# Kernel tuning notes

Hardware: AMD Instinct MI355X
Metric: run time of the kernel (lower is better)

The kernel has to match this reference:

```python
import jax, jax.numpy as jnp
import numpy as np

TAGSET = 50
T = TAGSET + 2      # tag_size incl START/STOP
START = T - 2       # START_TAG = -2
STOP = T - 1        # STOP_TAG = -1
NEG = -10000.0
B, S = 1024, 512


def _constrain(feats):
    # emissions to START/STOP are forbidden
    return feats.at[..., START].set(NEG).at[..., STOP].set(NEG)


def setup_inputs() -> dict:
    key = jax.random.key(0)
    kf, kl, kt, ktr = jax.random.split(key, 4)
    feats = jax.random.normal(kf, (B, S, T), jnp.float32)
    lengths = jax.random.randint(kl, (B,), S // 4, S + 1)
    mask = jnp.arange(S)[None, :] < lengths[:, None]  # bool prefix mask [B,S]
    tags = jax.random.randint(kt, (B, S), 0, TAGSET)
    # learned param: transitions with START/STOP constraints (as reset_parameters, but random base)
    transitions = 0.1 * jax.random.normal(ktr, (T, T), jnp.float32)
    transitions = transitions.at[:, START].set(NEG).at[STOP, :].set(NEG)
    return {"feats": feats, "mask": mask, "tags": tags, "transitions": transitions}


def reference(feats, mask, tags, transitions):
    del tags  # not used by Viterbi decode (forward)
    feats = _constrain(feats)
    b, s, t = feats.shape
    maskb = mask.astype(bool)
    lengths = jnp.maximum(maskb.sum(axis=1), 1)  # [B]

    alpha0 = transitions[START][None, :] + feats[:, 0]  # [B,T]

    def vstep(alpha, xs):
        f_t, m_t = xs  # [B,T], [B]
        scores = alpha[:, :, None] + transitions[None, :, :] + f_t[:, None, :]  # [B,T_prev,T_cur]
        nxt = scores.max(axis=1)
        bp = scores.argmax(axis=1).astype(jnp.int32)  # [B,T]
        alpha = jnp.where(m_t[:, None], nxt, alpha)
        return alpha, bp

    alpha, history = jax.lax.scan(
        vstep, alpha0, (feats[:, 1:].transpose(1, 0, 2), maskb[:, 1:].T)
    )  # history: [S-1,B,T]

    best_last = jnp.argmax(alpha + transitions[:, STOP][None, :], axis=1).astype(jnp.int32)  # [B]

    # pad so hist_pad[pos] == history[pos-1] for pos>=1
    hist_pad = jnp.concatenate([jnp.zeros((1, b, t), jnp.int32), history], axis=0)  # [S,B,T]

    def tb(ptr, xs):
        pos, bp = xs  # scalar, [B,T]
        ptr = jnp.where(pos == lengths - 1, best_last, ptr)
        tag = jnp.where(pos <= lengths - 1, ptr, 0)  # positions past length stay 0
        nxt = jnp.take_along_axis(bp, ptr[:, None], axis=1)[:, 0]
        ptr = jnp.where((pos >= 1) & (pos <= lengths - 1), nxt, ptr)
        return ptr, tag

    _, decoded = jax.lax.scan(tb, best_last, (jnp.arange(s), hist_pad), reverse=True)  # [S,B]
    return decoded.T  # [B,S] int32 best path
```

## Files before the change

kernel.cpp:

```cpp
#include <hip/hip_runtime.h>

#define TT 52
#define NT 50
#define START_TAG 50
#define STOP_TAG 51
#define BB 1024
#define SS 512
#define BPSTR 64

__device__ __forceinline__ int seq_len(const void* mask, int b, int j) {
    int cnt = 0;
    const unsigned* w = (const unsigned*)mask;
    unsigned w0 = w[0];
    unsigned w1 = w[1];
    if (w0 == 0x01010101u) {
        const unsigned char* m = (const unsigned char*)mask + (size_t)b * SS;
        for (int k = j; k < SS; k += 64) cnt += (m[k] != 0);
    } else if (w0 == 0x3f800000u) {
        const float* m = (const float*)mask + (size_t)b * SS;
        for (int k = j; k < SS; k += 64) cnt += (m[k] != 0.f);
    } else if (w1 == 1u) {
        const int* m = (const int*)mask + (size_t)b * SS;
        for (int k = j; k < SS; k += 64) cnt += (m[k] != 0);
    } else {
        const long long* m = (const long long*)mask + (size_t)b * SS;
        for (int k = j; k < SS; k += 64) cnt += (m[k] != 0);
    }
    for (int off = 32; off; off >>= 1) cnt += __shfl_xor(cnt, off, 64);
    return cnt > 0 ? cnt : 1;
}

#define DP_STEP(FREG, POSV)                                                       \
    {                                                                             \
        const int abits_ = __builtin_bit_cast(int, alpha);                        \
        float s_[NT];                                                             \
        _Pragma("unroll")                                                         \
        for (int i_ = 0; i_ < NT; ++i_)                                           \
            s_[i_] = __builtin_bit_cast(float,                                    \
                         __builtin_amdgcn_readlane(abits_, i_)) + tt[i_];         \
        float m_[17];                                                             \
        _Pragma("unroll")                                                         \
        for (int k_ = 0; k_ < 16; ++k_)                                           \
            m_[k_] = fmaxf(fmaxf(s_[3 * k_], s_[3 * k_ + 1]), s_[3 * k_ + 2]);    \
        m_[16] = fmaxf(s_[48], s_[49]);                                           \
        float n_[6];                                                              \
        _Pragma("unroll")                                                         \
        for (int k_ = 0; k_ < 5; ++k_)                                            \
            n_[k_] = fmaxf(fmaxf(m_[3 * k_], m_[3 * k_ + 1]), m_[3 * k_ + 2]);    \
        n_[5] = fmaxf(m_[15], m_[16]);                                            \
        float q0_ = fmaxf(fmaxf(n_[0], n_[1]), n_[2]);                            \
        float q1_ = fmaxf(fmaxf(n_[3], n_[4]), n_[5]);                            \
        float bv_ = fmaxf(q0_, q1_);                                              \
        wsb[(size_t)(POSV) * 64] = bv_;                                           \
        alpha = bv_ + (FREG);                                                     \
    }

#define FLD(P) fp[(size_t)((P) < SS ? (P) : SS - 1) * TT]

__global__ __launch_bounds__(64, 1) void crf_viterbi_fast(
    const float* __restrict__ feats,
    const void*  __restrict__ mask,
    const float* __restrict__ trans,
    float* __restrict__ ws,
    int* __restrict__ out)
{
    __shared__ float trans_lds[64 * 53];

    const int b = blockIdx.x;
    const int j = threadIdx.x;
    const int jc = j < NT ? j : NT - 1;
    const int jr = j * 53;

    for (int k = j; k < 64 * 53; k += 64) {
        int r = k / 53, c = k - r * 53;
        float v = -3.0e38f;
        if (r < NT && c < TT) v = trans[r * TT + c];
        trans_lds[k] = v;
    }

    const int len = seq_len(mask, b, j);

    float tt[NT];
#pragma unroll
    for (int i = 0; i < NT; ++i) tt[i] = trans[i * TT + j];

    const float* fp = feats + ((size_t)b * SS) * TT + jc;
    float* wsb = ws + ((size_t)b * SS) * 64 + j;
    const float bv0 = trans[START_TAG * TT + jc];
    float alpha = bv0 + fp[0];
    wsb[0] = bv0;

    float fA0 = FLD(1), fA1 = FLD(2), fA2 = FLD(3), fA3 = FLD(4);
    float fB0 = FLD(5), fB1 = FLD(6), fB2 = FLD(7), fB3 = FLD(8);

    int pos = 1;
    for (; pos + 7 < len; pos += 8) {
        DP_STEP(fA0, pos + 0)
        DP_STEP(fA1, pos + 1)
        DP_STEP(fA2, pos + 2)
        DP_STEP(fA3, pos + 3)
        fA0 = FLD(pos + 8);  fA1 = FLD(pos + 9);
        fA2 = FLD(pos + 10); fA3 = FLD(pos + 11);
        DP_STEP(fB0, pos + 4)
        DP_STEP(fB1, pos + 5)
        DP_STEP(fB2, pos + 6)
        DP_STEP(fB3, pos + 7)
        fB0 = FLD(pos + 12); fB1 = FLD(pos + 13);
        fB2 = FLD(pos + 14); fB3 = FLD(pos + 15);
    }
    if (pos < len) { DP_STEP(fA0, pos) ++pos; }
    if (pos < len) { DP_STEP(fA1, pos) ++pos; }
    if (pos < len) { DP_STEP(fA2, pos) ++pos; }
    if (pos < len) { DP_STEP(fA3, pos) ++pos; }
    if (pos < len) { DP_STEP(fB0, pos) ++pos; }
    if (pos < len) { DP_STEP(fB1, pos) ++pos; }
    if (pos < len) { DP_STEP(fB2, pos) ++pos; }

    float v = alpha + trans[jc * TT + STOP_TAG];
    if (j >= NT) v = -3.0e38f;
    int idx = j < NT ? j : 0;
    for (int off = 32; off; off >>= 1) {
        float vo = __shfl_xor(v, off, 64);
        int   io = __shfl_xor(idx, off, 64);
        if (vo > v || (vo == v && io < idx)) { v = vo; idx = io; }
    }

    __syncthreads();

    int ptr = idx;
    int* ob = out + (size_t)b * SS;
    ob[len - 1] = ptr;

    const float* wsr = ws + ((size_t)b * SS) * 64;
    const float* fbase = feats + ((size_t)b * SS) * TT;

    float bvs[4], fs[4];
    float bv_cur;
    {
        int r0 = len - 1;
        bv_cur = wsr[(size_t)r0 * 64 + j];
#pragma unroll
        for (int k = 0; k < 4; ++k) {
            int r = len - 2 - k; int rc = r < 0 ? 0 : r;
            bvs[k] = wsr[(size_t)rc * 64 + j];
            fs[k]  = fbase[(size_t)rc * TT + jc];
        }
    }

    int tpos = len - 1;

#define TB_STEP(k)                                                              \
    {                                                                           \
        float bv_prev = bvs[k];                                                 \
        float alpha_prev = bv_prev + fs[k];                                     \
        float cand = alpha_prev + trans_lds[jr + ptr];                          \
        float candm = (j < NT) ? cand : -3.0e38f;                               \
        float tgt = __builtin_bit_cast(float,                                   \
            __builtin_amdgcn_readlane(__builtin_bit_cast(int, bv_cur), ptr));   \
        unsigned long long bm = __ballot(candm == tgt);                         \
        ptr = __ffsll(bm) - 1;                                                  \
        --tpos;                                                                 \
        ob[tpos] = ptr;                                                         \
        bv_cur = bv_prev;                                                       \
        int rc = tpos - 4; rc = rc < 0 ? 0 : rc;                                \
        bvs[k] = wsr[(size_t)rc * 64 + j];                                      \
        fs[k]  = fbase[(size_t)rc * TT + jc];                                   \
    }

    while (tpos >= 4) {
        TB_STEP(0) TB_STEP(1) TB_STEP(2) TB_STEP(3)
    }
#pragma unroll
    for (int k = 0; k < 3; ++k) {
        if (tpos >= 1) TB_STEP(k)
    }
#undef TB_STEP

    for (int p = len + j; p < SS; p += 64) ob[p] = 0;
}

__global__ __launch_bounds__(64, 1) void crf_viterbi(
    const float* __restrict__ feats,
    const void*  __restrict__ mask,
    const float* __restrict__ trans,
    int* __restrict__ out)
{
    __shared__ unsigned char bp_sh[SS * BPSTR];

    const int b = blockIdx.x;
    const int j = threadIdx.x;
    const int jc = j < NT ? j : NT - 1;

    const int len = seq_len(mask, b, j);

    float tt[NT];
#pragma unroll
    for (int i = 0; i < NT; ++i) tt[i] = trans[i * TT + j];

    const float* fp = feats + ((size_t)b * SS) * TT + jc;
    float alpha = trans[START_TAG * TT + jc] + fp[0];
    float fnext = fp[TT];

    for (int pos = 1; pos < len; ++pos) {
        const float f = fnext;
        { int np = pos + 1 < SS ? pos + 1 : SS - 1; fnext = fp[(size_t)np * TT]; }

        float best[4] = { -3.0e38f, -3.0e38f, -3.0e38f, -3.0e38f };
        int   bidx[4] = { 0, 0, 0, 0 };
        const int abits = __builtin_bit_cast(int, alpha);
#pragma unroll
        for (int i = 0; i < NT; ++i) {
            int ab = __builtin_amdgcn_readlane(abits, i);
            float s = __builtin_bit_cast(float, ab) + tt[i];
            const int c = i & 3;
            if (s > best[c]) { best[c] = s; bidx[c] = i; }
        }
        float bv = best[0]; int bi = bidx[0];
        if (best[1] > bv || (best[1] == bv && bidx[1] < bi)) { bv = best[1]; bi = bidx[1]; }
        if (best[2] > bv || (best[2] == bv && bidx[2] < bi)) { bv = best[2]; bi = bidx[2]; }
        if (best[3] > bv || (best[3] == bv && bidx[3] < bi)) { bv = best[3]; bi = bidx[3]; }

        alpha = bv + f;
        bp_sh[pos * BPSTR + j] = (unsigned char)bi;
    }

    float v = alpha + trans[jc * TT + STOP_TAG];
    if (j >= NT) v = -3.0e38f;
    int idx = j < NT ? j : 0;
    for (int off = 32; off; off >>= 1) {
        float vo = __shfl_xor(v, off, 64);
        int   io = __shfl_xor(idx, off, 64);
        if (vo > v || (vo == v && io < idx)) { v = vo; idx = io; }
    }

    __syncthreads();

    int ptr = idx;
    int* ob = out + (size_t)b * SS;
    for (int pos = len - 1; pos >= 1; --pos) {
        if (j == 0) ob[pos] = ptr;
        ptr = (int)bp_sh[pos * BPSTR + ptr];
    }
    if (j == 0) ob[0] = ptr;

    for (int p = len + j; p < SS; p += 64) ob[p] = 0;
}

extern "C" void kernel_launch(void* const* d_in, const int* in_sizes, int n_in,
                              void* d_out, int out_size, void* d_ws, size_t ws_size,
                              hipStream_t stream) {
    const float* feats = (const float*)d_in[0];
    const void*  mask  = d_in[1];
    const float* trans = (const float*)d_in[3];
    int* out = (int*)d_out;

    const size_t need = (size_t)BB * SS * 64 * sizeof(float);
    if (ws_size >= need) {
        crf_viterbi_fast<<<dim3(BB), dim3(64), 0, stream>>>(feats, mask, trans,
                                                            (float*)d_ws, out);
    } else {
        crf_viterbi<<<dim3(BB), dim3(64), 0, stream>>>(feats, mask, trans, out);
    }
}
```

Baseline: 197.8 us.

## Split Viterbi max-reduction across four waves with LDS combine per step

Each block now runs four wavefronts. Each wave handles 13 of the 50 source tags in the per-step max, and the partial maxima are merged through double-buffered LDS with a workgroup barrier. The aim is to shorten the serial readlane/max chain per timestep and spread work over more SIMDs. In exchange it adds a barrier and an LDS round-trip to every step. Only wave 0 performs the traceback.

```diff
diff --git a/kernel.cpp b/kernel.cpp
--- a/kernel.cpp
+++ b/kernel.cpp
@@ -6,6 +6,8 @@
 #define STOP_TAG 51
 #define BB 1024
 #define SS 512
+#define NWAVE 4
+#define NSRC 13
 #define BPSTR 64
 
 __device__ __forceinline__ int seq_len(const void* mask, int b, int j) {
@@ -33,45 +35,49 @@
 #define DP_STEP(FREG, POSV)                                                       \
     {                                                                             \
         const int abits_ = __builtin_bit_cast(int, alpha);                        \
-        float s_[NT];                                                             \
+        float s_[NSRC];                                                           \
         _Pragma("unroll")                                                         \
-        for (int i_ = 0; i_ < NT; ++i_)                                           \
+        for (int i_ = 0; i_ < NSRC; ++i_)                                         \
             s_[i_] = __builtin_bit_cast(float,                                    \
-                         __builtin_amdgcn_readlane(abits_, i_)) + tt[i_];         \
-        float m_[17];                                                             \
-        _Pragma("unroll")                                                         \
-        for (int k_ = 0; k_ < 16; ++k_)                                           \
-            m_[k_] = fmaxf(fmaxf(s_[3 * k_], s_[3 * k_ + 1]), s_[3 * k_ + 2]);    \
-        m_[16] = fmaxf(s_[48], s_[49]);                                           \
-        float n_[6];                                                              \
-        _Pragma("unroll")                                                         \
-        for (int k_ = 0; k_ < 5; ++k_)                                            \
-            n_[k_] = fmaxf(fmaxf(m_[3 * k_], m_[3 * k_ + 1]), m_[3 * k_ + 2]);    \
-        n_[5] = fmaxf(m_[15], m_[16]);                                            \
-        float q0_ = fmaxf(fmaxf(n_[0], n_[1]), n_[2]);                            \
-        float q1_ = fmaxf(fmaxf(n_[3], n_[4]), n_[5]);                            \
-        float bv_ = fmaxf(q0_, q1_);                                              \
-        wsb[(size_t)(POSV) * 64] = bv_;                                           \
+                         __builtin_amdgcn_readlane(abits_, wbase + i_)) + tt[i_]; \
+        float m0_ = fmaxf(fmaxf(s_[0], s_[1]), s_[2]);                            \
+        float m1_ = fmaxf(fmaxf(s_[3], s_[4]), s_[5]);                            \
+        float m2_ = fmaxf(fmaxf(s_[6], s_[7]), s_[8]);                            \
+        float m3_ = fmaxf(fmaxf(s_[9], s_[10]), s_[11]);                          \
+        float t0_ = fmaxf(fmaxf(m0_, m1_), m2_);                                  \
+        float t1_ = fmaxf(m3_, s_[12]);                                           \
+        float pm_ = fmaxf(t0_, t1_);                                              \
+        ((float*)&pm_lds[(POSV) & 1][j])[w] = pm_;                                \
+        asm volatile("s_waitcnt lgkmcnt(0)" ::: "memory");                        \
+        __builtin_amdgcn_s_barrier();                                             \
+        asm volatile("" ::: "memory");                                            \
+        float4 q_ = pm_lds[(POSV) & 1][j];                                        \
+        float bv_ = fmaxf(fmaxf(fmaxf(q_.x, q_.y), q_.z), q_.w);                  \
+        if (w == 0) wsb[(size_t)(POSV) * 64] = bv_;                               \
         alpha = bv_ + (FREG);                                                     \
     }
 
 #define FLD(P) fp[(size_t)((P) < SS ? (P) : SS - 1) * TT]
 
-__global__ __launch_bounds__(64, 1) void crf_viterbi_fast(
+__global__ __launch_bounds__(256, 4) void crf_viterbi_fast(
     const float* __restrict__ feats,
     const void*  __restrict__ mask,
     const float* __restrict__ trans,
     float* __restrict__ ws,
     int* __restrict__ out)
 {
-    __shared__ float trans_lds[64 * 53];
-
-    const int b = blockIdx.x;
-    const int j = threadIdx.x;
-    const int jc = j < NT ? j : NT - 1;
-    const int jr = j * 53;
-
-    for (int k = j; k < 64 * 53; k += 64) {
+    __shared__ float  trans_lds[64 * 53];
+    __shared__ float4 pm_lds[2][64];
+
+    const int b   = blockIdx.x;
+    const int tid = threadIdx.x;
+    const int w   = tid >> 6;
+    const int j   = tid & 63;
+    const int jc  = j < NT ? j : NT - 1;
+    const int jr  = j * 53;
+    const int wbase = w * NSRC;
+
+    for (int k = tid; k < 64 * 53; k += 256) {
         int r = k / 53, c = k - r * 53;
         float v = -3.0e38f;
         if (r < NT && c < TT) v = trans[r * TT + c];
@@ -80,15 +86,18 @@
 
     const int len = seq_len(mask, b, j);
 
-    float tt[NT];
-#pragma unroll
-    for (int i = 0; i < NT; ++i) tt[i] = trans[i * TT + j];
-
-    const float* fp = feats + ((size_t)b * SS) * TT + jc;
-    float* wsb = ws + ((size_t)b * SS) * 64 + j;
+    float tt[NSRC];
+#pragma unroll
+    for (int i = 0; i < NSRC; ++i) {
+        int src = wbase + i;
+        tt[i] = (src < NT) ? trans[src * TT + j] : -3.0e38f;
+    }
+
+    const float* fp  = feats + ((size_t)b * SS) * TT + jc;
+    float*       wsb = ws + ((size_t)b * SS) * 64 + j;
     const float bv0 = trans[START_TAG * TT + jc];
     float alpha = bv0 + fp[0];
-    wsb[0] = bv0;
+    if (w == 0) wsb[0] = bv0;
 
     float fA0 = FLD(1), fA1 = FLD(2), fA2 = FLD(3), fA3 = FLD(4);
     float fB0 = FLD(5), fB1 = FLD(6), fB2 = FLD(7), fB3 = FLD(8);
@@ -116,6 +125,8 @@
     if (pos < len) { DP_STEP(fB1, pos) ++pos; }
     if (pos < len) { DP_STEP(fB2, pos) ++pos; }
 
+    if (w != 0) return;
+
     float v = alpha + trans[jc * TT + STOP_TAG];
     if (j >= NT) v = -3.0e38f;
     int idx = j < NT ? j : 0;
@@ -125,13 +136,11 @@
         if (vo > v || (vo == v && io < idx)) { v = vo; idx = io; }
     }
 
-    __syncthreads();
-
     int ptr = idx;
     int* ob = out + (size_t)b * SS;
     ob[len - 1] = ptr;
 
-    const float* wsr = ws + ((size_t)b * SS) * 64;
+    const float* wsr   = ws + ((size_t)b * SS) * 64;
     const float* fbase = feats + ((size_t)b * SS) * TT;
 
     float bvs[4], fs[4];
@@ -256,8 +265,8 @@
 
     const size_t need = (size_t)BB * SS * 64 * sizeof(float);
     if (ws_size >= need) {
-        crf_viterbi_fast<<<dim3(BB), dim3(64), 0, stream>>>(feats, mask, trans,
-                                                            (float*)d_ws, out);
+        crf_viterbi_fast<<<dim3(BB), dim3(256), 0, stream>>>(feats, mask, trans,
+                                                             (float*)d_ws, out);
     } else {
         crf_viterbi<<<dim3(BB), dim3(64), 0, stream>>>(feats, mask, trans, out);
     }
```

New measurement: 322.8 us. 1.63x slower.
